# Kernel optimization log

Hardware: AMD Instinct MI355X
Metric: run time of the kernel (lower is better)

## Reference

```python
import jax, jax.numpy as jnp
import numpy as np

SCALE = 100.0          # sigmoid sharpness used as soft comparator in long division
PRECISION_BITS = 16    # number of long-division iterations (ReciprocalFFN layers)


def setup_inputs() -> dict:
    key = jax.random.key(0)
    kq, kk, kv = jax.random.split(key, 3)
    B, D, N = 8192, 1024, 2048
    return {
        "query": jax.random.normal(kq, (B, D), dtype=jnp.float32),
        "keys": jax.random.normal(kk, (N, D), dtype=jnp.float32),
        "values": jax.random.normal(kv, (N, D), dtype=jnp.float32),
    }


def _reciprocal_scan(divisor):
    """16-step non-restoring long division computing ~1/divisor.

    Mirrors ReciprocalFFN: state = (remainder, quotient), remainder starts at 1,
    each step: doubled = 2*r; step = sigmoid(SCALE*(doubled - d));
    r' = doubled - d*step; q' = q + 2^{-(i+1)} * step.
    divisor: (B, 1) -> returns quotient (B, 1).
    """
    bit_weights = 2.0 ** -(jnp.arange(PRECISION_BITS, dtype=jnp.float32) + 1.0)

    def body(carry, w):
        r, q = carry
        doubled = r * 2.0
        step = jax.nn.sigmoid(SCALE * (doubled - divisor))
        return (doubled - divisor * step, q + w * step), None

    init = (jnp.ones_like(divisor), jnp.zeros_like(divisor))
    (_, quotient), _ = jax.lax.scan(body, init, bit_weights)
    return quotient


def reference(query, keys, values):
    # Baked-mode forward: QK scores -> softmax1 with FFN long-division reciprocal
    # -> weighted sum of values.
    scale = keys.shape[-1] ** -0.5
    scores = jnp.einsum("bd,nd->bn", query, keys) * scale          # (B, N)
    exps = jnp.exp(scores - jnp.max(scores, axis=-1, keepdims=True))
    sum_exp = 1.0 + jnp.sum(exps, axis=-1, keepdims=True)           # (B, 1)
    reciprocal = _reciprocal_scan(sum_exp)                          # (B, 1)
    weights = exps * reciprocal                                     # (B, N)
    return jnp.einsum("bn,nd->bd", weights, values)                 # (B, D)
```

## Files before the change

kernel.cpp:

```cpp
#include <hip/hip_runtime.h>
#include <hip/hip_bf16.h>
#include <stdint.h>
#include <math.h>

#define BQ   8192
#define DIM  1024
#define NK   2048

typedef unsigned short u16;
using f32x4  = __attribute__((ext_vector_type(4))) float;
using bf16x8 = __attribute__((ext_vector_type(8))) __bf16;
using f16x8  = __attribute__((ext_vector_type(8))) _Float16;
using u16x4  = __attribute__((ext_vector_type(4))) unsigned short;
using u16x8  = __attribute__((ext_vector_type(8))) unsigned short;

#define EXP_BIAS 4.0f


__device__ __forceinline__ u16 f2bf(float f) {
    uint32_t u = __float_as_uint(f);
    u += 0x7FFFu + ((u >> 16) & 1u);
    return (u16)(u >> 16);
}

__device__ __forceinline__ u16 f2h(float f) {
    _Float16 h = (_Float16)f;
    return __builtin_bit_cast(unsigned short, h);
}

__device__ __forceinline__ void gload_lds16(const void* g, void* l) {
    __builtin_amdgcn_global_load_lds(
        (const __attribute__((address_space(1))) void*)g,
        (__attribute__((address_space(3))) void*)l,
        16, 0, 0);
}

template<bool F16>
__device__ __forceinline__ f32x4 mfmaT(u16x8 a, u16x8 b, f32x4 c) {
    if constexpr (F16)
        return __builtin_amdgcn_mfma_f32_16x16x32_f16(
            __builtin_bit_cast(f16x8, a), __builtin_bit_cast(f16x8, b), c, 0, 0, 0);
    else
        return __builtin_amdgcn_mfma_f32_16x16x32_bf16(
            __builtin_bit_cast(bf16x8, a), __builtin_bit_cast(bf16x8, b), c, 0, 0, 0);
}


__global__ __launch_bounds__(256)
void cvt_all(const float* __restrict__ Q, const float* __restrict__ K,
             const float* __restrict__ V,
             u16* __restrict__ Qb, u16* __restrict__ Kb, u16* __restrict__ VT,
             int n4Q, int n4T, int nCvt) {
    const int b = blockIdx.x;
    if (b < nCvt) {
        int i = b * 256 + threadIdx.x;
        if (i >= n4T) return;
        const float* src; u16* dst; int j;
        if (i < n4Q) { src = Q; dst = Qb; j = i; }
        else         { src = K; dst = Kb; j = i - n4Q; }
        f32x4 v = reinterpret_cast<const f32x4*>(src)[j];
        u16x4 o;
        o.x = f2bf(v[0]); o.y = f2bf(v[1]); o.z = f2bf(v[2]); o.w = f2bf(v[3]);
        reinterpret_cast<u16x4*>(dst)[j] = o;
    } else {
        __shared__ float tile[32][33];
        const int id = b - nCvt;
        const int d0 = (id & (DIM / 32 - 1)) * 32;
        const int n0 = (id / (DIM / 32)) * 32;
        const int tx = threadIdx.x & 31;
        const int ty = threadIdx.x >> 5;
#pragma unroll
        for (int i = 0; i < 4; ++i)
            tile[ty + i * 8][tx] = V[(size_t)(n0 + ty + i * 8) * DIM + d0 + tx];
        __syncthreads();
#pragma unroll
        for (int i = 0; i < 4; ++i)
            VT[(size_t)(d0 + ty + i * 8) * NK + n0 + tx] = f2h(tile[tx][ty + i * 8]);
    }
}


template<int BN, bool F16, bool EXPOUT, bool STATS, bool HASF, typename OT>
__global__ __launch_bounds__(512, 2)
void gemm256(const u16* __restrict__ A, const u16* __restrict__ B, OT* __restrict__ C,
             const float* __restrict__ rowFactor,
             float* __restrict__ pSum, float* __restrict__ pMax,
             int K, int lda, int ldb, int ldc, float scale, int nbn) {
    constexpr int WTN  = BN / 4;
    constexpr int NREP = BN / 64;
    constexpr int NH   = NREP / 2;
    constexpr int BCALLS = (BN == 256) ? 4 : 2;

    __shared__ u16 As[2][256 * 64];
    __shared__ u16 Bs[2][BN * 64];

    const int tid  = threadIdx.x;
    const int wave = tid >> 6;
    const int lane = tid & 63;
    const int wr = wave >> 2;
    const int wc = wave & 3;

    int id = blockIdx.x;
    const int cpx = gridDim.x >> 3;
    id = (id & 7) * cpx + (id >> 3);
    const int bm = id / nbn;
    const int bn = id % nbn;

    const int lsub  = lane >> 3;
    const int lslot = lane & 7;
    const int srcColEl = ((lslot ^ lsub) << 3);

    const int aRow0 = wr * 128 + wc * 32;
    int bRow0;
    if constexpr (BN == 256) bRow0 = (wc >> 1) * 128 + (wr * 2 + (wc & 1)) * 32;
    else                     bRow0 = wave * 16;

    const u16* aSrc = A + (size_t)(bm * 256 + aRow0 + lsub) * lda + srcColEl;
    const u16* bSrc = B + (size_t)(bn * BN  + bRow0 + lsub) * ldb + srcColEl;

    f32x4 acc[8][NREP] = {};

    const int NT = K >> 6;

    auto STAGE = [&](int buf, int kt) {
        const size_t ko = (size_t)kt * 64;
#pragma unroll
        for (int c2 = 0; c2 < 4; ++c2)
            gload_lds16(aSrc + (size_t)c2 * 8 * lda + ko, &As[buf][(aRow0 + c2 * 8) * 64]);
#pragma unroll
        for (int c2 = 0; c2 < BCALLS; ++c2)
            gload_lds16(bSrc + (size_t)c2 * 8 * ldb + ko, &Bs[buf][(bRow0 + c2 * 8) * 64]);
    };

    auto LDA_frag = [&](const char* base, int m, int kk) -> u16x8 {
        int r   = wr * 128 + m * 16 + (lane & 15);
        int off = r * 128 + (((kk * 64) + ((lane >> 4) << 4)) ^ ((lane & 7) << 4));
        return *reinterpret_cast<const u16x8*>(base + off);
    };
    auto LDB_frag = [&](const char* base, int n, int kk) -> u16x8 {
        int r   = wc * WTN + n * 16 + (lane & 15);
        int off = r * 128 + (((kk * 64) + ((lane >> 4) << 4)) ^ ((lane & 7) << 4));
        return *reinterpret_cast<const u16x8*>(base + off);
    };

    STAGE(0, 0);
    __syncthreads();

    int cbuf = 0;
    for (int t = 0; t < NT; ++t) {
        if (t + 1 < NT) STAGE(cbuf ^ 1, t + 1);
        __builtin_amdgcn_sched_barrier(0);

        const char* aB = (const char*)&As[cbuf][0];
        const char* bB = (const char*)&Bs[cbuf][0];

        u16x8 af[4][2];
        u16x8 bf0[NH][2], bf1[NH][2];

#pragma unroll
        for (int mi = 0; mi < 4; ++mi) { af[mi][0] = LDA_frag(aB, mi, 0); af[mi][1] = LDA_frag(aB, mi, 1); }
#pragma unroll
        for (int ni = 0; ni < NH; ++ni) { bf0[ni][0] = LDB_frag(bB, ni, 0); bf0[ni][1] = LDB_frag(bB, ni, 1); }
#pragma unroll
        for (int mi = 0; mi < 4; ++mi)
#pragma unroll
            for (int ni = 0; ni < NH; ++ni) {
                acc[mi][ni] = mfmaT<F16>(af[mi][0], bf0[ni][0], acc[mi][ni]);
                acc[mi][ni] = mfmaT<F16>(af[mi][1], bf0[ni][1], acc[mi][ni]);
            }

#pragma unroll
        for (int ni = 0; ni < NH; ++ni) { bf1[ni][0] = LDB_frag(bB, NH + ni, 0); bf1[ni][1] = LDB_frag(bB, NH + ni, 1); }
#pragma unroll
        for (int mi = 0; mi < 4; ++mi)
#pragma unroll
            for (int ni = 0; ni < NH; ++ni) {
                acc[mi][NH + ni] = mfmaT<F16>(af[mi][0], bf1[ni][0], acc[mi][NH + ni]);
                acc[mi][NH + ni] = mfmaT<F16>(af[mi][1], bf1[ni][1], acc[mi][NH + ni]);
            }

#pragma unroll
        for (int mi = 0; mi < 4; ++mi) { af[mi][0] = LDA_frag(aB, 4 + mi, 0); af[mi][1] = LDA_frag(aB, 4 + mi, 1); }
#pragma unroll
        for (int mi = 0; mi < 4; ++mi)
#pragma unroll
            for (int ni = 0; ni < NH; ++ni) {
                acc[4 + mi][NH + ni] = mfmaT<F16>(af[mi][0], bf1[ni][0], acc[4 + mi][NH + ni]);
                acc[4 + mi][NH + ni] = mfmaT<F16>(af[mi][1], bf1[ni][1], acc[4 + mi][NH + ni]);
            }

#pragma unroll
        for (int mi = 0; mi < 4; ++mi)
#pragma unroll
            for (int ni = 0; ni < NH; ++ni) {
                acc[4 + mi][ni] = mfmaT<F16>(af[mi][0], bf0[ni][0], acc[4 + mi][ni]);
                acc[4 + mi][ni] = mfmaT<F16>(af[mi][1], bf0[ni][1], acc[4 + mi][ni]);
            }

        __syncthreads();
        cbuf ^= 1;
    }

    const int col0 = bn * BN + wc * WTN + (lane & 15);
    const int row0 = bm * 256 + wr * 128 + ((lane >> 4) << 2);
#pragma unroll
    for (int m = 0; m < 8; ++m) {
#pragma unroll
        for (int j = 0; j < 4; ++j) {
            const int row = row0 + m * 16 + j;
            float rf = 1.0f;
            if constexpr (HASF) rf = rowFactor[row];
            OT* cp = C + (size_t)row * ldc + col0;
            float psum = 0.f, pmx = 0.f;
#pragma unroll
            for (int n = 0; n < NREP; ++n) {
                float v = acc[m][n][j] * scale;
                if constexpr (EXPOUT) v = expf(v - EXP_BIAS);
                if constexpr (STATS) { psum += v; pmx = fmaxf(pmx, v); }
                cp[n * 16] = (OT)(v * rf);
            }
            if constexpr (STATS) {
#pragma unroll
                for (int off = 1; off < 16; off <<= 1) {
                    psum += __shfl_xor(psum, off);
                    pmx   = fmaxf(pmx, __shfl_xor(pmx, off));
                }
                if ((lane & 15) == 0) {
                    const int slot = bn * 4 + wc;
                    pSum[(size_t)row * 32 + slot] = psum;
                    pMax[(size_t)row * 32 + slot] = pmx;
                }
            }
        }
    }
}


__global__ __launch_bounds__(128)
void finalize_factor(const float* __restrict__ pSum, const float* __restrict__ pMax,
                     float* __restrict__ factor) {
    const int row = blockIdx.x * 128 + threadIdx.x;
    const f32x4* ps = reinterpret_cast<const f32x4*>(pSum + (size_t)row * 32);
    const f32x4* pm = reinterpret_cast<const f32x4*>(pMax + (size_t)row * 32);

    float T = 0.f, mx = 0.f;
#pragma unroll
    for (int i = 0; i < 8; ++i) {
        f32x4 a = ps[i];
        f32x4 b = pm[i];
        T  += (a[0] + a[1]) + (a[2] + a[3]);
        mx  = fmaxf(mx, fmaxf(fmaxf(b[0], b[1]), fmaxf(b[2], b[3])));
    }

    const float d = 1.0f + T / mx;

    float r = 1.0f, q = 0.0f, w = 0.5f;
#pragma unroll
    for (int i = 0; i < 16; ++i) {
        float doubled = 2.0f * r;
        float st = 1.0f / (1.0f + expf(-100.0f * (doubled - d)));
        r = doubled - d * st;
        q += w * st;
        w *= 0.5f;
    }

    factor[row] = q / mx;
}


extern "C" void kernel_launch(void* const* d_in, const int* in_sizes, int n_in,
                              void* d_out, int out_size, void* d_ws, size_t ws_size,
                              hipStream_t stream) {
    const float* Q = (const float*)d_in[0];
    const float* K = (const float*)d_in[1];
    const float* V = (const float*)d_in[2];
    float* out = (float*)d_out;

    char* ws = (char*)d_ws;
    u16*   Qb     = (u16*)(ws);
    u16*   Kb     = (u16*)(ws + (16u << 20));
    u16*   VhT    = (u16*)(ws + (20u << 20));
    u16*   E      = (u16*)(ws + (24u << 20));
    float* pSum   = (float*)(ws + (56u << 20));
    float* pMax   = (float*)(ws + (57u << 20));
    float* factor = (float*)(ws + (58u << 20));

    {
        int n4Q = BQ * DIM / 4;
        int n4T = n4Q + NK * DIM / 4;
        int nCvt = (n4T + 255) / 256;
        int nTrs = (DIM / 32) * (NK / 32);
        cvt_all<<<nCvt + nTrs, 256, 0, stream>>>(Q, K, V, Qb, Kb, VhT, n4Q, n4T, nCvt);
    }

    gemm256<256, false, true, true, false, _Float16>
        <<<(BQ / 256) * (NK / 256), 512, 0, stream>>>(
        Qb, Kb, (_Float16*)E, nullptr, pSum, pMax, DIM, DIM, DIM, NK, 0.03125f, NK / 256);

    finalize_factor<<<BQ / 128, 128, 0, stream>>>(pSum, pMax, factor);

    gemm256<128, true, false, false, true, float>
        <<<(BQ / 256) * (DIM / 128), 512, 0, stream>>>(
        E, VhT, out, factor, nullptr, nullptr, NK, NK, NK, DIM, 1.0f, DIM / 128);
}
```

Measured before the change: 99.37 us.

## Use single-buffered 128x128 tile GEMM for QK score stage

Adds a new 256-thread GEMM kernel with 128x128 output tiles and a single LDS buffer, and uses it for the QK^T + exp + row-stats stage in place of the double-buffered 256x256 kernel. The smaller tile gives four times as many workgroups and allows higher occupancy (3 blocks per CU). The cost is lower operand reuse per tile and no overlap of global loads with MFMA compute, since the kernel syncs twice per K step. Partial stats still use 32 slots per row (nbn*2 = 16*2).

```diff
diff --git a/kernel.cpp b/kernel.cpp
--- a/kernel.cpp
+++ b/kernel.cpp
@@ -80,6 +80,113 @@
 }
 
 
+template<bool F16, bool EXPOUT, bool STATS, bool HASF, typename OT>
+__global__ __launch_bounds__(256, 3)
+void gemm128s(const u16* __restrict__ A, const u16* __restrict__ B, OT* __restrict__ C,
+              const float* __restrict__ rowFactor,
+              float* __restrict__ pSum, float* __restrict__ pMax,
+              int K, int lda, int ldb, int ldc, float scale, int nbn) {
+    __shared__ u16 As[128 * 64];
+    __shared__ u16 Bs[128 * 64];
+
+    const int tid  = threadIdx.x;
+    const int wave = tid >> 6;
+    const int lane = tid & 63;
+    const int wr = wave >> 1;
+    const int wc = wave & 1;
+
+    int id = blockIdx.x;
+    const int cpx = gridDim.x >> 3;
+    id = (id & 7) * cpx + (id >> 3);
+    const int bm = id / nbn;
+    const int bn = id % nbn;
+
+    const int lsub  = lane >> 3;
+    const int lslot = lane & 7;
+    const int srcColEl = ((lslot ^ lsub) << 3);
+
+    const u16* aSrc = A + (size_t)(bm * 128 + wave * 8 + lsub) * lda + srcColEl;
+    const u16* bSrc = B + (size_t)(bn * 128 + wave * 8 + lsub) * ldb + srcColEl;
+    const int dst0 = (wave * 8) * 64;
+
+    const int fr = lane & 15;
+    auto LDA_frag = [&](int m, int kk) -> u16x8 {
+        int r   = wr * 64 + m * 16 + fr;
+        int off = r * 128 + ((kk * 64 + ((lane >> 4) << 4)) ^ ((lane & 7) << 4));
+        return *reinterpret_cast<const u16x8*>(
+            reinterpret_cast<const char*>(&As[0]) + off);
+    };
+    auto LDB_frag = [&](int n, int kk) -> u16x8 {
+        int r   = wc * 64 + n * 16 + fr;
+        int off = r * 128 + ((kk * 64 + ((lane >> 4) << 4)) ^ ((lane & 7) << 4));
+        return *reinterpret_cast<const u16x8*>(
+            reinterpret_cast<const char*>(&Bs[0]) + off);
+    };
+
+    f32x4 acc[4][4] = {};
+    const int NT = K >> 6;
+
+    for (int t = 0; t < NT; ++t) {
+        const size_t ko = (size_t)t * 64;
+#pragma unroll
+        for (int c = 0; c < 4; ++c) {
+            gload_lds16(aSrc + (size_t)(c * 32) * lda + ko, &As[dst0 + c * 32 * 64]);
+            gload_lds16(bSrc + (size_t)(c * 32) * ldb + ko, &Bs[dst0 + c * 32 * 64]);
+        }
+        __syncthreads();
+
+#pragma unroll
+        for (int kk = 0; kk < 2; ++kk) {
+            u16x8 af[4], bf[4];
+#pragma unroll
+            for (int m = 0; m < 4; ++m) af[m] = LDA_frag(m, kk);
+#pragma unroll
+            for (int n = 0; n < 4; ++n) bf[n] = LDB_frag(n, kk);
+#pragma unroll
+            for (int m = 0; m < 4; ++m)
+#pragma unroll
+                for (int n = 0; n < 4; ++n)
+                    acc[m][n] = mfmaT<F16>(af[m], bf[n], acc[m][n]);
+        }
+
+        __syncthreads();
+    }
+
+    const int col0 = bn * 128 + wc * 64 + fr;
+    const int row0 = bm * 128 + wr * 64 + ((lane >> 4) << 2);
+#pragma unroll
+    for (int m = 0; m < 4; ++m) {
+#pragma unroll
+        for (int j = 0; j < 4; ++j) {
+            const int row = row0 + m * 16 + j;
+            float rf = 1.0f;
+            if constexpr (HASF) rf = rowFactor[row];
+            OT* cp = C + (size_t)row * ldc + col0;
+            float psum = 0.f, pmx = 0.f;
+#pragma unroll
+            for (int n = 0; n < 4; ++n) {
+                float v = acc[m][n][j] * scale;
+                if constexpr (EXPOUT) v = expf(v - EXP_BIAS);
+                if constexpr (STATS) { psum += v; pmx = fmaxf(pmx, v); }
+                cp[n * 16] = (OT)(v * rf);
+            }
+            if constexpr (STATS) {
+#pragma unroll
+                for (int off = 1; off < 16; off <<= 1) {
+                    psum += __shfl_xor(psum, off);
+                    pmx   = fmaxf(pmx, __shfl_xor(pmx, off));
+                }
+                if ((lane & 15) == 0) {
+                    const int slot = bn * 2 + wc;
+                    pSum[(size_t)row * 32 + slot] = psum;
+                    pMax[(size_t)row * 32 + slot] = pmx;
+                }
+            }
+        }
+    }
+}
+
+
 template<int BN, bool F16, bool EXPOUT, bool STATS, bool HASF, typename OT>
 __global__ __launch_bounds__(512, 2)
 void gemm256(const u16* __restrict__ A, const u16* __restrict__ B, OT* __restrict__ C,
@@ -293,9 +400,9 @@
         cvt_all<<<nCvt + nTrs, 256, 0, stream>>>(Q, K, V, Qb, Kb, VhT, n4Q, n4T, nCvt);
     }
 
-    gemm256<256, false, true, true, false, _Float16>
-        <<<(BQ / 256) * (NK / 256), 512, 0, stream>>>(
-        Qb, Kb, (_Float16*)E, nullptr, pSum, pMax, DIM, DIM, DIM, NK, 0.03125f, NK / 256);
+    gemm128s<false, true, true, false, _Float16>
+        <<<(BQ / 128) * (NK / 128), 256, 0, stream>>>(
+        Qb, Kb, (_Float16*)E, nullptr, pSum, pMax, DIM, DIM, DIM, NK, 0.03125f, NK / 128);
 
     finalize_factor<<<BQ / 128, 128, 0, stream>>>(pSum, pMax, factor);
 
```

New measurement: 102.2 us. 1.03x slower.
